# Kernel optimization log

Measured on AMD Instinct MI355X. Metric: run time of the kernel, lower is better.

Reference implementation:

```python
import jax, jax.numpy as jnp
import numpy as np

MODEL_DIM = 1024
HEADS = 16
HEAD_DIM = MODEL_DIM // HEADS
OUT_DIM = 1024
B, S = 2, 2048


def setup_inputs() -> dict:
    key = jax.random.key(0)
    ks = jax.random.split(key, 10)
    scale = 1.0 / np.sqrt(MODEL_DIM)
    return {
        "query": jax.random.normal(ks[0], (B, S, MODEL_DIM), dtype=jnp.float32),
        "bank": jax.random.normal(ks[1], (B, S, MODEL_DIM), dtype=jnp.float32),
        "Wq": jax.random.normal(ks[2], (MODEL_DIM, MODEL_DIM), dtype=jnp.float32) * scale,
        "bq": jnp.zeros((MODEL_DIM,), dtype=jnp.float32),
        "Wk": jax.random.normal(ks[3], (MODEL_DIM, MODEL_DIM), dtype=jnp.float32) * scale,
        "bk": jnp.zeros((MODEL_DIM,), dtype=jnp.float32),
        "Wv": jax.random.normal(ks[4], (MODEL_DIM, MODEL_DIM), dtype=jnp.float32) * scale,
        "bv": jnp.zeros((MODEL_DIM,), dtype=jnp.float32),
        "Wo": jax.random.normal(ks[5], (OUT_DIM, MODEL_DIM), dtype=jnp.float32) * scale,
        "bo": jnp.zeros((OUT_DIM,), dtype=jnp.float32),
    }


def _split_heads(x):
    # [B, S, D] -> [B, H, S, hd]
    b, s, _ = x.shape
    return x.reshape(b, s, HEADS, HEAD_DIM).transpose(0, 2, 1, 3)


def reference(query, bank, Wq, bq, Wk, bk, Wv, bv, Wo, bo):
    # Linear projections (torch Linear: x @ W.T + b)
    q = _split_heads(query @ Wq.T + bq)  # [B,H,Sq,hd]
    k = _split_heads(bank @ Wk.T + bk)   # [B,H,Sk,hd]
    v = _split_heads(bank @ Wv.T + bv)   # [B,H,Sk,hd]
    score_scale = jnp.sqrt(jnp.float32(HEAD_DIM))
    scores = jnp.einsum("bhqd,bhkd->bhqk", q / score_scale, k)  # [B,H,Sq,Sk]
    attn = jax.nn.softmax(scores, axis=-1)
    # dropout is identity in eval-mode reference
    ctx = jnp.einsum("bhqk,bhkd->bhqd", attn, v)  # [B,H,Sq,hd]
    b, h, sq, hd = ctx.shape
    ctx = ctx.transpose(0, 2, 1, 3).reshape(b, sq, MODEL_DIM)
    return ctx @ Wo.T + bo
```

## Files before the change

kernel.cpp:

```cpp
#include <hip/hip_runtime.h>


#define BDIM   2
#define SDIM   2048
#define DDIM   1024
#define HEADS  16
#define HD     64
#define MROWS  (BDIM * SDIM)

typedef float  f32x4  __attribute__((ext_vector_type(4)));
typedef __bf16 bf16x8 __attribute__((ext_vector_type(8)));
typedef __bf16 bf16x4 __attribute__((ext_vector_type(4)));
typedef unsigned u32x4 __attribute__((ext_vector_type(4)));

#define QSCALE 0.18033688011112042f

__device__ __forceinline__ void stage16(const void* g, void* l) {
    __builtin_amdgcn_global_load_lds((const __attribute__((address_space(1))) void*)g,
                                     (__attribute__((address_space(3))) void*)l,
                                     16, 0, 0);
}

__device__ __forceinline__ float vexp2(float x) {
    float r;
    asm("v_exp_f32 %0, %1" : "=v"(r) : "v"(x));
    return r;
}
__device__ __forceinline__ unsigned pk2(float lo, float hi) {
    unsigned r;
    asm("v_cvt_pk_bf16_f32 %0, %1, %2" : "=v"(r) : "v"(lo), "v"(hi));
    return r;
}

__global__ __launch_bounds__(256) void cvt_all(
    const float* __restrict__ q, const float* __restrict__ bank,
    const float* __restrict__ Wq, const float* __restrict__ Wk,
    const float* __restrict__ Wv, const float* __restrict__ Wo,
    __bf16* __restrict__ xq, __bf16* __restrict__ xkv,
    __bf16* __restrict__ wq, __bf16* __restrict__ wk,
    __bf16* __restrict__ wv, __bf16* __restrict__ wo) {
    const int i = blockIdx.x * 256 + threadIdx.x;
    const float* in;
    __bf16* out;
    int off;
    if (i < 524288)       { in = q;    out = xq;  off = i; }
    else if (i < 1048576) { in = bank; out = xkv; off = i - 524288; }
    else {
        const int j = i - 1048576;
        const int sel = j >> 17;
        off = j & 131071;
        in  = (sel == 0) ? Wq : (sel == 1) ? Wk : (sel == 2) ? Wv : Wo;
        out = (sel == 0) ? wq : (sel == 1) ? wk : (sel == 2) ? wv : wo;
    }
    const float4* p = (const float4*)in;
    float4 a = p[2 * off];
    float4 c = p[2 * off + 1];
    bf16x8 o;
    o[0] = (__bf16)a.x; o[1] = (__bf16)a.y; o[2] = (__bf16)a.z; o[3] = (__bf16)a.w;
    o[4] = (__bf16)c.x; o[5] = (__bf16)c.y; o[6] = (__bf16)c.z; o[7] = (__bf16)c.w;
    *(bf16x8*)(out + 8 * off) = o;
}

template <int MODE>
__global__ __launch_bounds__(256) void gemm_bt(
    const __bf16* __restrict__ Aq, const __bf16* __restrict__ Akv,
    const __bf16* __restrict__ W0, const __bf16* __restrict__ W1,
    const __bf16* __restrict__ W2,
    const float* __restrict__ b0, const float* __restrict__ b1,
    const float* __restrict__ b2,
    __bf16* __restrict__ Qo, __bf16* __restrict__ Ko, __bf16* __restrict__ Vo,
    float* __restrict__ Fo) {
    constexpr int NF = (MODE == 2) ? 2 : 4;
    constexpr int NCOL = NF * 32;
    __shared__ __align__(16) __bf16 ldsA[128 * 32];
    __shared__ __align__(16) __bf16 ldsB[(NCOL)*32];

    const int t = threadIdx.x;
    const int l = t & 63;
    const int w = t >> 6;
    const int z = (MODE == 0) ? (int)blockIdx.z : 0;

    const __bf16* A  = (MODE == 0 && z != 0) ? Akv : Aq;
    const __bf16* Wm = (z == 0) ? W0 : (z == 1 ? W1 : W2);
    const float*  bias = (z == 0) ? b0 : (z == 1 ? b1 : b2);

    const int row0 = blockIdx.x * 128;
    const int col0 = blockIdx.y * NCOL;

    const int sg = (t & 3) ^ ((t >> 3) & 3);
    const __bf16* ga = A  + (size_t)(row0 + (t >> 2)) * DDIM + sg * 8;
    const __bf16* gb = Wm + (size_t)(col0 + (t >> 2)) * DDIM + sg * 8;
    __bf16* la = ldsA + (t & ~63) * 8;
    __bf16* lb = ldsB + (t & ~63) * 8;

    const int wm = w >> 1, wn = w & 1;
    const int i15 = l & 15;
    const int q4 = l >> 4;
    const int gx = q4 ^ ((i15 >> 1) & 3);

    const int aoff = (wm * 64 + i15) * 32 + gx * 8;
    const int boff = (wn * (NF * 16) + i15) * 32 + gx * 8;

    f32x4 acc[4][NF] = {};

    for (int kb = 0; kb < DDIM; kb += 32) {
        __syncthreads();
        stage16(ga + kb,             la);
        stage16(ga + kb + 64 * DDIM, la + 2048);
        stage16(gb + kb,             lb);
        if constexpr (MODE == 0)
            stage16(gb + kb + 64 * DDIM, lb + 2048);
        __syncthreads();

        bf16x8 af[4], bf[NF];
#pragma unroll
        for (int m = 0; m < 4; ++m) af[m] = *(const bf16x8*)(ldsA + aoff + m * 16 * 32);
#pragma unroll
        for (int n = 0; n < NF; ++n) bf[n] = *(const bf16x8*)(ldsB + boff + n * 16 * 32);
#pragma unroll
        for (int m = 0; m < 4; ++m)
#pragma unroll
            for (int n = 0; n < NF; ++n)
                acc[m][n] = __builtin_amdgcn_mfma_f32_16x16x32_bf16(af[m], bf[n], acc[m][n], 0, 0, 0);
    }

#pragma unroll
    for (int m = 0; m < 4; ++m) {
        const int rbase = row0 + wm * 64 + m * 16 + (l >> 4) * 4;
#pragma unroll
        for (int n = 0; n < NF; ++n) {
            const int col = col0 + wn * (NF * 16) + n * 16 + (l & 15);
            const float bv = bias[col];
            if constexpr (MODE == 0) {
                const int hh = col >> 6, dd = col & 63;
#pragma unroll
                for (int j = 0; j < 4; ++j) {
                    const int r = rbase + j;
                    const int b = r >> 11, s = r & 2047;
                    const float v = acc[m][n][j] + bv;
                    if (z == 0) {
                        Qo[(((b * HEADS + hh) * SDIM + s) << 6) + dd] = (__bf16)(v * QSCALE);
                    } else if (z == 1) {
                        Ko[(((b * HEADS + hh) * SDIM + s) << 6) + dd] = (__bf16)v;
                    } else {
                        Vo[(((b * HEADS + hh) * HD + dd) << 11) + s] = (__bf16)v;
                    }
                }
            } else {
#pragma unroll
                for (int j = 0; j < 4; ++j) {
                    Fo[(size_t)(rbase + j) * DDIM + col] = acc[m][n][j] + bv;
                }
            }
        }
    }
}

__global__ __launch_bounds__(512) void attn_fwd(const __bf16* __restrict__ Qb,
                                                const __bf16* __restrict__ Kb,
                                                const __bf16* __restrict__ Vtb,
                                                __bf16* __restrict__ Cb) {
    __shared__ __align__(16) __bf16 ldsK[2][2][64 * 64];
    __shared__ __align__(16) __bf16 ldsV[2][2][64 * 64];

    const int t = threadIdx.x;
    const int l = t & 63;
    const int w = t >> 6;
    const int i15 = l & 15;
    const int q4 = l >> 4;

    const int bid  = blockIdx.x;
    const int xcd  = bid & 7;
    const int wloc = bid >> 3;
    const int bh   = xcd * 4 + (wloc >> 4);
    const int qb   = wloc & 15;
    const int b    = bh >> 4;
    const int h    = bh & 15;
    const size_t base = (size_t)bh * SDIM * HD;
    const int q0 = qb * 128;

    const __bf16* qp = Qb + base + (size_t)(q0 + w * 16 + i15) * HD + q4 * 8;
    const bf16x8 qf0 = *(const bf16x8*)(qp);
    const bf16x8 qf1 = *(const bf16x8*)(qp + 32);

    const int r0 = t >> 3;
    const int sl = (t & 7) ^ (r0 & 7);
    const int sig0 = ((r0 >> 5) << 5) | (((r0 >> 2) & 3) << 3)
                   | (((r0 >> 4) & 1) << 2) | (r0 & 3);
    const __bf16* gk = Kb  + base + (size_t)sig0 * HD + sl * 8;
    const __bf16* gv = Vtb + base + (size_t)r0 * SDIM + sl * 8;
    const int wb = (t & ~63) * 8;

    const int xr = i15 & 7;
    int off[4][2];
#pragma unroll
    for (int n = 0; n < 4; ++n)
#pragma unroll
        for (int hh = 0; hh < 2; ++hh)
            off[n][hh] = (n * 16 + i15) * 64 + (((hh * 4 + q4) ^ xr) << 3);

    bf16x8 ones;
#pragma unroll
    for (int j = 0; j < 8; ++j) ones[j] = (__bf16)1.0f;

    f32x4 c[4] = {};
    f32x4 lsum = {};

    stage16(gk,           &ldsK[0][0][wb]);
    stage16(gk + 64 * HD, &ldsK[0][1][wb]);
    stage16(gv,           &ldsV[0][0][wb]);
    stage16(gv + 64,      &ldsV[0][1][wb]);

#pragma unroll 2
    for (int r = 0; r < SDIM / 128; ++r) {
        const int bb = r & 1;
        __syncthreads();

        if (r + 1 < SDIM / 128) {
            const int s0 = (r + 1) * 128;
            stage16(gk + (size_t)s0 * HD,        &ldsK[bb ^ 1][0][wb]);
            stage16(gk + (size_t)(s0 + 64) * HD, &ldsK[bb ^ 1][1][wb]);
            stage16(gv + s0,                     &ldsV[bb ^ 1][0][wb]);
            stage16(gv + s0 + 64,                &ldsV[bb ^ 1][1][wb]);
        }

        const __bf16* lk0 = &ldsK[bb][0][0];
        const __bf16* lk1 = &ldsK[bb][1][0];
        const __bf16* lv0 = &ldsV[bb][0][0];
        const __bf16* lv1 = &ldsV[bb][1][0];

        f32x4 sA[4] = {}, sB[4] = {};
        __builtin_amdgcn_s_setprio(1);
#pragma unroll
        for (int n = 0; n < 4; ++n) {
            bf16x8 k0 = *(const bf16x8*)(lk0 + off[n][0]);
            bf16x8 k1 = *(const bf16x8*)(lk0 + off[n][1]);
            sA[n] = __builtin_amdgcn_mfma_f32_16x16x32_bf16(k0, qf0, sA[n], 0, 0, 0);
            sA[n] = __builtin_amdgcn_mfma_f32_16x16x32_bf16(k1, qf1, sA[n], 0, 0, 0);
        }
#pragma unroll
        for (int n = 0; n < 4; ++n) {
            bf16x8 k0 = *(const bf16x8*)(lk1 + off[n][0]);
            bf16x8 k1 = *(const bf16x8*)(lk1 + off[n][1]);
            sB[n] = __builtin_amdgcn_mfma_f32_16x16x32_bf16(k0, qf0, sB[n], 0, 0, 0);
            sB[n] = __builtin_amdgcn_mfma_f32_16x16x32_bf16(k1, qf1, sB[n], 0, 0, 0);
        }
        __builtin_amdgcn_s_setprio(0);

#pragma unroll
        for (int n = 0; n < 4; ++n)
#pragma unroll
            for (int j = 0; j < 4; ++j) {
                sA[n][j] = vexp2(sA[n][j]);
                sB[n][j] = vexp2(sB[n][j]);
            }

        u32x4 pw0, pw1, pw2, pw3;
        pw0[0] = pk2(sA[0][0], sA[0][1]); pw0[1] = pk2(sA[0][2], sA[0][3]);
        pw0[2] = pk2(sA[1][0], sA[1][1]); pw0[3] = pk2(sA[1][2], sA[1][3]);
        pw1[0] = pk2(sA[2][0], sA[2][1]); pw1[1] = pk2(sA[2][2], sA[2][3]);
        pw1[2] = pk2(sA[3][0], sA[3][1]); pw1[3] = pk2(sA[3][2], sA[3][3]);
        pw2[0] = pk2(sB[0][0], sB[0][1]); pw2[1] = pk2(sB[0][2], sB[0][3]);
        pw2[2] = pk2(sB[1][0], sB[1][1]); pw2[3] = pk2(sB[1][2], sB[1][3]);
        pw3[0] = pk2(sB[2][0], sB[2][1]); pw3[1] = pk2(sB[2][2], sB[2][3]);
        pw3[2] = pk2(sB[3][0], sB[3][1]); pw3[3] = pk2(sB[3][2], sB[3][3]);
        const bf16x8 paA0 = __builtin_bit_cast(bf16x8, pw0);
        const bf16x8 paB0 = __builtin_bit_cast(bf16x8, pw1);
        const bf16x8 paA1 = __builtin_bit_cast(bf16x8, pw2);
        const bf16x8 paB1 = __builtin_bit_cast(bf16x8, pw3);

        __builtin_amdgcn_s_setprio(1);
        lsum = __builtin_amdgcn_mfma_f32_16x16x32_bf16(ones, paA0, lsum, 0, 0, 0);
        lsum = __builtin_amdgcn_mfma_f32_16x16x32_bf16(ones, paB0, lsum, 0, 0, 0);
        lsum = __builtin_amdgcn_mfma_f32_16x16x32_bf16(ones, paA1, lsum, 0, 0, 0);
        lsum = __builtin_amdgcn_mfma_f32_16x16x32_bf16(ones, paB1, lsum, 0, 0, 0);
#pragma unroll
        for (int n2 = 0; n2 < 4; ++n2) {
            bf16x8 v0 = *(const bf16x8*)(lv0 + off[n2][0]);
            bf16x8 v1 = *(const bf16x8*)(lv0 + off[n2][1]);
            c[n2] = __builtin_amdgcn_mfma_f32_16x16x32_bf16(v0, paA0, c[n2], 0, 0, 0);
            c[n2] = __builtin_amdgcn_mfma_f32_16x16x32_bf16(v1, paB0, c[n2], 0, 0, 0);
            bf16x8 u0 = *(const bf16x8*)(lv1 + off[n2][0]);
            bf16x8 u1 = *(const bf16x8*)(lv1 + off[n2][1]);
            c[n2] = __builtin_amdgcn_mfma_f32_16x16x32_bf16(u0, paA1, c[n2], 0, 0, 0);
            c[n2] = __builtin_amdgcn_mfma_f32_16x16x32_bf16(u1, paB1, c[n2], 0, 0, 0);
        }
        __builtin_amdgcn_s_setprio(0);
    }

    const float inv = 1.0f / lsum[0];
    const int q = q0 + w * 16 + i15;
#pragma unroll
    for (int n2 = 0; n2 < 4; ++n2) {
        bf16x4 o;
#pragma unroll
        for (int j = 0; j < 4; ++j) o[j] = (__bf16)(c[n2][j] * inv);
        *(bf16x4*)(Cb + (size_t)(b * SDIM + q) * DDIM + h * HD + n2 * 16 + q4 * 4) = o;
    }
}

extern "C" void kernel_launch(void* const* d_in, const int* in_sizes, int n_in,
                              void* d_out, int out_size, void* d_ws, size_t ws_size,
                              hipStream_t stream) {
    const float* query = (const float*)d_in[0];
    const float* bank  = (const float*)d_in[1];
    const float* Wq = (const float*)d_in[2];
    const float* bq = (const float*)d_in[3];
    const float* Wk = (const float*)d_in[4];
    const float* bk = (const float*)d_in[5];
    const float* Wv = (const float*)d_in[6];
    const float* bv = (const float*)d_in[7];
    const float* Wo = (const float*)d_in[8];
    const float* bo = (const float*)d_in[9];
    float* out = (float*)d_out;

    char* ws = (char*)d_ws;
    __bf16* xq  = (__bf16*)(ws);
    __bf16* xkv = (__bf16*)(ws + (8u  << 20));
    __bf16* wq  = (__bf16*)(ws + (16u << 20));
    __bf16* wk  = (__bf16*)(ws + (18u << 20));
    __bf16* wv  = (__bf16*)(ws + (20u << 20));
    __bf16* wo  = (__bf16*)(ws + (22u << 20));
    __bf16* qbuf = (__bf16*)(ws + (24u << 20));
    __bf16* kbuf = (__bf16*)(ws + (32u << 20));
    __bf16* vtbuf = (__bf16*)(ws + (40u << 20));
    __bf16* ctx = xq;

    cvt_all<<<6144, 256, 0, stream>>>(query, bank, Wq, Wk, Wv, Wo,
                                      xq, xkv, wq, wk, wv, wo);

    gemm_bt<0><<<dim3(32, 8, 3), 256, 0, stream>>>(
        xq, xkv, wq, wk, wv, bq, bk, bv, qbuf, kbuf, vtbuf, nullptr);

    attn_fwd<<<512, 512, 0, stream>>>(qbuf, kbuf, vtbuf, ctx);

    gemm_bt<2><<<dim3(32, 16, 1), 256, 0, stream>>>(
        ctx, nullptr, wo, nullptr, nullptr, bo, nullptr, nullptr,
        nullptr, nullptr, nullptr, out);
}
```

Baseline: 112.4 us.

## Have each attention wave process two 16-row query tiles with half the threads

The attention kernel now launches 256 threads per block instead of 512. Each wave handles two 16-row query tiles (rows q and q+64), so every K and V fragment read from LDS feeds twice as many MFMAs. Staging is split into twice as many 16-byte loads per thread to fill the same 128-key tiles. This cuts LDS read traffic per unit of compute but doubles accumulator and score registers per wave and halves the waves per block, which may reduce latency hiding.

```diff
diff --git a/kernel.cpp b/kernel.cpp
--- a/kernel.cpp
+++ b/kernel.cpp
@@ -156,7 +156,7 @@
     }
 }
 
-__global__ __launch_bounds__(512) void attn_fwd(const __bf16* __restrict__ Qb,
+__global__ __launch_bounds__(256) void attn_fwd(const __bf16* __restrict__ Qb,
                                                 const __bf16* __restrict__ Kb,
                                                 const __bf16* __restrict__ Vtb,
                                                 __bf16* __restrict__ Cb) {
@@ -180,13 +180,14 @@
     const int q0 = qb * 128;
 
     const __bf16* qp = Qb + base + (size_t)(q0 + w * 16 + i15) * HD + q4 * 8;
-    const bf16x8 qf0 = *(const bf16x8*)(qp);
-    const bf16x8 qf1 = *(const bf16x8*)(qp + 32);
+    const bf16x8 qf00 = *(const bf16x8*)(qp);
+    const bf16x8 qf01 = *(const bf16x8*)(qp + 32);
+    const bf16x8 qf10 = *(const bf16x8*)(qp + 64 * HD);
+    const bf16x8 qf11 = *(const bf16x8*)(qp + 64 * HD + 32);
 
     const int r0 = t >> 3;
     const int sl = (t & 7) ^ (r0 & 7);
-    const int sig0 = ((r0 >> 5) << 5) | (((r0 >> 2) & 3) << 3)
-                   | (((r0 >> 4) & 1) << 2) | (r0 & 3);
+    const int sig0 = (((r0 >> 2) & 3) << 3) | (((r0 >> 4) & 1) << 2) | (r0 & 3);
     const __bf16* gk = Kb  + base + (size_t)sig0 * HD + sl * 8;
     const __bf16* gv = Vtb + base + (size_t)r0 * SDIM + sl * 8;
     const int wb = (t & ~63) * 8;
@@ -203,13 +204,17 @@
 #pragma unroll
     for (int j = 0; j < 8; ++j) ones[j] = (__bf16)1.0f;
 
-    f32x4 c[4] = {};
-    f32x4 lsum = {};
-
-    stage16(gk,           &ldsK[0][0][wb]);
-    stage16(gk + 64 * HD, &ldsK[0][1][wb]);
-    stage16(gv,           &ldsV[0][0][wb]);
-    stage16(gv + 64,      &ldsV[0][1][wb]);
+    f32x4 c0[4] = {}, c1[4] = {};
+    f32x4 ls0 = {}, ls1 = {};
+
+    stage16(gk,                       &ldsK[0][0][wb]);
+    stage16(gk + 32 * HD,             &ldsK[0][0][wb + 2048]);
+    stage16(gk + 64 * HD,             &ldsK[0][1][wb]);
+    stage16(gk + 96 * HD,             &ldsK[0][1][wb + 2048]);
+    stage16(gv,                       &ldsV[0][0][wb]);
+    stage16(gv + (size_t)32 * SDIM,   &ldsV[0][0][wb + 2048]);
+    stage16(gv + 64,                  &ldsV[0][1][wb]);
+    stage16(gv + 64 + (size_t)32 * SDIM, &ldsV[0][1][wb + 2048]);
 
 #pragma unroll 2
     for (int r = 0; r < SDIM / 128; ++r) {
@@ -218,10 +223,14 @@
 
         if (r + 1 < SDIM / 128) {
             const int s0 = (r + 1) * 128;
-            stage16(gk + (size_t)s0 * HD,        &ldsK[bb ^ 1][0][wb]);
-            stage16(gk + (size_t)(s0 + 64) * HD, &ldsK[bb ^ 1][1][wb]);
-            stage16(gv + s0,                     &ldsV[bb ^ 1][0][wb]);
-            stage16(gv + s0 + 64,                &ldsV[bb ^ 1][1][wb]);
+            stage16(gk + (size_t)(s0)*HD,          &ldsK[bb ^ 1][0][wb]);
+            stage16(gk + (size_t)(s0 + 32) * HD,   &ldsK[bb ^ 1][0][wb + 2048]);
+            stage16(gk + (size_t)(s0 + 64) * HD,   &ldsK[bb ^ 1][1][wb]);
+            stage16(gk + (size_t)(s0 + 96) * HD,   &ldsK[bb ^ 1][1][wb + 2048]);
+            stage16(gv + s0,                       &ldsV[bb ^ 1][0][wb]);
+            stage16(gv + s0 + (size_t)32 * SDIM,   &ldsV[bb ^ 1][0][wb + 2048]);
+            stage16(gv + s0 + 64,                  &ldsV[bb ^ 1][1][wb]);
+            stage16(gv + s0 + 64 + (size_t)32 * SDIM, &ldsV[bb ^ 1][1][wb + 2048]);
         }
 
         const __bf16* lk0 = &ldsK[bb][0][0];
@@ -229,21 +238,25 @@
         const __bf16* lv0 = &ldsV[bb][0][0];
         const __bf16* lv1 = &ldsV[bb][1][0];
 
-        f32x4 sA[4] = {}, sB[4] = {};
+        f32x4 sA[4] = {}, sB[4] = {}, sC[4] = {}, sD[4] = {};
         __builtin_amdgcn_s_setprio(1);
 #pragma unroll
         for (int n = 0; n < 4; ++n) {
             bf16x8 k0 = *(const bf16x8*)(lk0 + off[n][0]);
             bf16x8 k1 = *(const bf16x8*)(lk0 + off[n][1]);
-            sA[n] = __builtin_amdgcn_mfma_f32_16x16x32_bf16(k0, qf0, sA[n], 0, 0, 0);
-            sA[n] = __builtin_amdgcn_mfma_f32_16x16x32_bf16(k1, qf1, sA[n], 0, 0, 0);
+            sA[n] = __builtin_amdgcn_mfma_f32_16x16x32_bf16(k0, qf00, sA[n], 0, 0, 0);
+            sC[n] = __builtin_amdgcn_mfma_f32_16x16x32_bf16(k0, qf10, sC[n], 0, 0, 0);
+            sA[n] = __builtin_amdgcn_mfma_f32_16x16x32_bf16(k1, qf01, sA[n], 0, 0, 0);
+            sC[n] = __builtin_amdgcn_mfma_f32_16x16x32_bf16(k1, qf11, sC[n], 0, 0, 0);
         }
 #pragma unroll
         for (int n = 0; n < 4; ++n) {
             bf16x8 k0 = *(const bf16x8*)(lk1 + off[n][0]);
             bf16x8 k1 = *(const bf16x8*)(lk1 + off[n][1]);
-            sB[n] = __builtin_amdgcn_mfma_f32_16x16x32_bf16(k0, qf0, sB[n], 0, 0, 0);
-            sB[n] = __builtin_amdgcn_mfma_f32_16x16x32_bf16(k1, qf1, sB[n], 0, 0, 0);
+            sB[n] = __builtin_amdgcn_mfma_f32_16x16x32_bf16(k0, qf00, sB[n], 0, 0, 0);
+            sD[n] = __builtin_amdgcn_mfma_f32_16x16x32_bf16(k0, qf10, sD[n], 0, 0, 0);
+            sB[n] = __builtin_amdgcn_mfma_f32_16x16x32_bf16(k1, qf01, sB[n], 0, 0, 0);
+            sD[n] = __builtin_amdgcn_mfma_f32_16x16x32_bf16(k1, qf11, sD[n], 0, 0, 0);
         }
         __builtin_amdgcn_s_setprio(0);
 
@@ -253,49 +266,76 @@
             for (int j = 0; j < 4; ++j) {
                 sA[n][j] = vexp2(sA[n][j]);
                 sB[n][j] = vexp2(sB[n][j]);
+                sC[n][j] = vexp2(sC[n][j]);
+                sD[n][j] = vexp2(sD[n][j]);
             }
 
-        u32x4 pw0, pw1, pw2, pw3;
-        pw0[0] = pk2(sA[0][0], sA[0][1]); pw0[1] = pk2(sA[0][2], sA[0][3]);
-        pw0[2] = pk2(sA[1][0], sA[1][1]); pw0[3] = pk2(sA[1][2], sA[1][3]);
-        pw1[0] = pk2(sA[2][0], sA[2][1]); pw1[1] = pk2(sA[2][2], sA[2][3]);
-        pw1[2] = pk2(sA[3][0], sA[3][1]); pw1[3] = pk2(sA[3][2], sA[3][3]);
-        pw2[0] = pk2(sB[0][0], sB[0][1]); pw2[1] = pk2(sB[0][2], sB[0][3]);
-        pw2[2] = pk2(sB[1][0], sB[1][1]); pw2[3] = pk2(sB[1][2], sB[1][3]);
-        pw3[0] = pk2(sB[2][0], sB[2][1]); pw3[1] = pk2(sB[2][2], sB[2][3]);
-        pw3[2] = pk2(sB[3][0], sB[3][1]); pw3[3] = pk2(sB[3][2], sB[3][3]);
-        const bf16x8 paA0 = __builtin_bit_cast(bf16x8, pw0);
-        const bf16x8 paB0 = __builtin_bit_cast(bf16x8, pw1);
-        const bf16x8 paA1 = __builtin_bit_cast(bf16x8, pw2);
-        const bf16x8 paB1 = __builtin_bit_cast(bf16x8, pw3);
+        u32x4 w0, w1, w2, w3, w4, w5, w6, w7;
+        w0[0] = pk2(sA[0][0], sA[0][1]); w0[1] = pk2(sA[0][2], sA[0][3]);
+        w0[2] = pk2(sA[1][0], sA[1][1]); w0[3] = pk2(sA[1][2], sA[1][3]);
+        w1[0] = pk2(sA[2][0], sA[2][1]); w1[1] = pk2(sA[2][2], sA[2][3]);
+        w1[2] = pk2(sA[3][0], sA[3][1]); w1[3] = pk2(sA[3][2], sA[3][3]);
+        w2[0] = pk2(sB[0][0], sB[0][1]); w2[1] = pk2(sB[0][2], sB[0][3]);
+        w2[2] = pk2(sB[1][0], sB[1][1]); w2[3] = pk2(sB[1][2], sB[1][3]);
+        w3[0] = pk2(sB[2][0], sB[2][1]); w3[1] = pk2(sB[2][2], sB[2][3]);
+        w3[2] = pk2(sB[3][0], sB[3][1]); w3[3] = pk2(sB[3][2], sB[3][3]);
+        w4[0] = pk2(sC[0][0], sC[0][1]); w4[1] = pk2(sC[0][2], sC[0][3]);
+        w4[2] = pk2(sC[1][0], sC[1][1]); w4[3] = pk2(sC[1][2], sC[1][3]);
+        w5[0] = pk2(sC[2][0], sC[2][1]); w5[1] = pk2(sC[2][2], sC[2][3]);
+        w5[2] = pk2(sC[3][0], sC[3][1]); w5[3] = pk2(sC[3][2], sC[3][3]);
+        w6[0] = pk2(sD[0][0], sD[0][1]); w6[1] = pk2(sD[0][2], sD[0][3]);
+        w6[2] = pk2(sD[1][0], sD[1][1]); w6[3] = pk2(sD[1][2], sD[1][3]);
+        w7[0] = pk2(sD[2][0], sD[2][1]); w7[1] = pk2(sD[2][2], sD[2][3]);
+        w7[2] = pk2(sD[3][0], sD[3][1]); w7[3] = pk2(sD[3][2], sD[3][3]);
+        const bf16x8 pA = __builtin_bit_cast(bf16x8, w0);
+        const bf16x8 pB = __builtin_bit_cast(bf16x8, w1);
+        const bf16x8 pC = __builtin_bit_cast(bf16x8, w2);
+        const bf16x8 pD = __builtin_bit_cast(bf16x8, w3);
+        const bf16x8 rA = __builtin_bit_cast(bf16x8, w4);
+        const bf16x8 rB = __builtin_bit_cast(bf16x8, w5);
+        const bf16x8 rC = __builtin_bit_cast(bf16x8, w6);
+        const bf16x8 rD = __builtin_bit_cast(bf16x8, w7);
 
         __builtin_amdgcn_s_setprio(1);
-        lsum = __builtin_amdgcn_mfma_f32_16x16x32_bf16(ones, paA0, lsum, 0, 0, 0);
-        lsum = __builtin_amdgcn_mfma_f32_16x16x32_bf16(ones, paB0, lsum, 0, 0, 0);
-        lsum = __builtin_amdgcn_mfma_f32_16x16x32_bf16(ones, paA1, lsum, 0, 0, 0);
-        lsum = __builtin_amdgcn_mfma_f32_16x16x32_bf16(ones, paB1, lsum, 0, 0, 0);
+        ls0 = __builtin_amdgcn_mfma_f32_16x16x32_bf16(ones, pA, ls0, 0, 0, 0);
+        ls0 = __builtin_amdgcn_mfma_f32_16x16x32_bf16(ones, pB, ls0, 0, 0, 0);
+        ls0 = __builtin_amdgcn_mfma_f32_16x16x32_bf16(ones, pC, ls0, 0, 0, 0);
+        ls0 = __builtin_amdgcn_mfma_f32_16x16x32_bf16(ones, pD, ls0, 0, 0, 0);
+        ls1 = __builtin_amdgcn_mfma_f32_16x16x32_bf16(ones, rA, ls1, 0, 0, 0);
+        ls1 = __builtin_amdgcn_mfma_f32_16x16x32_bf16(ones, rB, ls1, 0, 0, 0);
+        ls1 = __builtin_amdgcn_mfma_f32_16x16x32_bf16(ones, rC, ls1, 0, 0, 0);
+        ls1 = __builtin_amdgcn_mfma_f32_16x16x32_bf16(ones, rD, ls1, 0, 0, 0);
 #pragma unroll
         for (int n2 = 0; n2 < 4; ++n2) {
             bf16x8 v0 = *(const bf16x8*)(lv0 + off[n2][0]);
             bf16x8 v1 = *(const bf16x8*)(lv0 + off[n2][1]);
-            c[n2] = __builtin_amdgcn_mfma_f32_16x16x32_bf16(v0, paA0, c[n2], 0, 0, 0);
-            c[n2] = __builtin_amdgcn_mfma_f32_16x16x32_bf16(v1, paB0, c[n2], 0, 0, 0);
+            c0[n2] = __builtin_amdgcn_mfma_f32_16x16x32_bf16(v0, pA, c0[n2], 0, 0, 0);
+            c1[n2] = __builtin_amdgcn_mfma_f32_16x16x32_bf16(v0, rA, c1[n2], 0, 0, 0);
+            c0[n2] = __builtin_amdgcn_mfma_f32_16x16x32_bf16(v1, pB, c0[n2], 0, 0, 0);
+            c1[n2] = __builtin_amdgcn_mfma_f32_16x16x32_bf16(v1, rB, c1[n2], 0, 0, 0);
             bf16x8 u0 = *(const bf16x8*)(lv1 + off[n2][0]);
             bf16x8 u1 = *(const bf16x8*)(lv1 + off[n2][1]);
-            c[n2] = __builtin_amdgcn_mfma_f32_16x16x32_bf16(u0, paA1, c[n2], 0, 0, 0);
-            c[n2] = __builtin_amdgcn_mfma_f32_16x16x32_bf16(u1, paB1, c[n2], 0, 0, 0);
+            c0[n2] = __builtin_amdgcn_mfma_f32_16x16x32_bf16(u0, pC, c0[n2], 0, 0, 0);
+            c1[n2] = __builtin_amdgcn_mfma_f32_16x16x32_bf16(u0, rC, c1[n2], 0, 0, 0);
+            c0[n2] = __builtin_amdgcn_mfma_f32_16x16x32_bf16(u1, pD, c0[n2], 0, 0, 0);
+            c1[n2] = __builtin_amdgcn_mfma_f32_16x16x32_bf16(u1, rD, c1[n2], 0, 0, 0);
         }
         __builtin_amdgcn_s_setprio(0);
     }
 
-    const float inv = 1.0f / lsum[0];
+    const float inv0 = 1.0f / ls0[0];
+    const float inv1 = 1.0f / ls1[0];
     const int q = q0 + w * 16 + i15;
 #pragma unroll
     for (int n2 = 0; n2 < 4; ++n2) {
-        bf16x4 o;
-#pragma unroll
-        for (int j = 0; j < 4; ++j) o[j] = (__bf16)(c[n2][j] * inv);
-        *(bf16x4*)(Cb + (size_t)(b * SDIM + q) * DDIM + h * HD + n2 * 16 + q4 * 4) = o;
+        bf16x4 oA, oB;
+#pragma unroll
+        for (int j = 0; j < 4; ++j) {
+            oA[j] = (__bf16)(c0[n2][j] * inv0);
+            oB[j] = (__bf16)(c1[n2][j] * inv1);
+        }
+        *(bf16x4*)(Cb + (size_t)(b * SDIM + q) * DDIM + h * HD + n2 * 16 + q4 * 4) = oA;
+        *(bf16x4*)(Cb + (size_t)(b * SDIM + q + 64) * DDIM + h * HD + n2 * 16 + q4 * 4) = oB;
     }
 }
 
@@ -332,7 +372,7 @@
     gemm_bt<0><<<dim3(32, 8, 3), 256, 0, stream>>>(
         xq, xkv, wq, wk, wv, bq, bk, bv, qbuf, kbuf, vtbuf, nullptr);
 
-    attn_fwd<<<512, 512, 0, stream>>>(qbuf, kbuf, vtbuf, ctx);
+    attn_fwd<<<512, 256, 0, stream>>>(qbuf, kbuf, vtbuf, ctx);
 
     gemm_bt<2><<<dim3(32, 16, 1), 256, 0, stream>>>(
         ctx, nullptr, wo, nullptr, nullptr, bo, nullptr, nullptr,
```

Measured after the change: 112.2 us. No clear change (-0.1%).

## Fuse fp32-to-bf16 activation conversion into QKV projection GEMM

Applied to the files above, without the earlier changes.

The standalone pass that converted query and bank activations to bf16 is removed. The QKV GEMM now stages fp32 activation tiles straight into LDS with a new swizzle and packs them to bf16 in registers before the MFMA. Only the weights are still pre-converted. This avoids a full read and write of both activation tensors, at the cost of twice the LDS footprint and staging traffic for the A operand plus extra pack instructions, and the z=1 and z=2 blocks each re-read the fp32 bank.

```diff
diff --git a/kernel.cpp b/kernel.cpp
--- a/kernel.cpp
+++ b/kernel.cpp
@@ -32,38 +32,31 @@
     return r;
 }
 
-__global__ __launch_bounds__(256) void cvt_all(
-    const float* __restrict__ q, const float* __restrict__ bank,
-    const float* __restrict__ Wq, const float* __restrict__ Wk,
-    const float* __restrict__ Wv, const float* __restrict__ Wo,
-    __bf16* __restrict__ xq, __bf16* __restrict__ xkv,
-    __bf16* __restrict__ wq, __bf16* __restrict__ wk,
-    __bf16* __restrict__ wv, __bf16* __restrict__ wo) {
-    const int i = blockIdx.x * 256 + threadIdx.x;
-    const float* in;
-    __bf16* out;
-    int off;
-    if (i < 524288)       { in = q;    out = xq;  off = i; }
-    else if (i < 1048576) { in = bank; out = xkv; off = i - 524288; }
-    else {
-        const int j = i - 1048576;
-        const int sel = j >> 17;
-        off = j & 131071;
-        in  = (sel == 0) ? Wq : (sel == 1) ? Wk : (sel == 2) ? Wv : Wo;
-        out = (sel == 0) ? wq : (sel == 1) ? wk : (sel == 2) ? wv : wo;
-    }
+__global__ __launch_bounds__(256) void cvt8w(const float* __restrict__ w0,
+                                             const float* __restrict__ w1,
+                                             const float* __restrict__ w2,
+                                             const float* __restrict__ w3,
+                                             __bf16* __restrict__ o0,
+                                             __bf16* __restrict__ o1,
+                                             __bf16* __restrict__ o2,
+                                             __bf16* __restrict__ o3) {
+    const int sel = blockIdx.x >> 9;
+    const float* in  = (sel == 0) ? w0 : (sel == 1) ? w1 : (sel == 2) ? w2 : w3;
+    __bf16*      out = (sel == 0) ? o0 : (sel == 1) ? o1 : (sel == 2) ? o2 : o3;
+    int i = (blockIdx.x & 511) * 256 + threadIdx.x;
     const float4* p = (const float4*)in;
-    float4 a = p[2 * off];
-    float4 c = p[2 * off + 1];
+    float4 a = p[2 * i];
+    float4 c = p[2 * i + 1];
     bf16x8 o;
     o[0] = (__bf16)a.x; o[1] = (__bf16)a.y; o[2] = (__bf16)a.z; o[3] = (__bf16)a.w;
     o[4] = (__bf16)c.x; o[5] = (__bf16)c.y; o[6] = (__bf16)c.z; o[7] = (__bf16)c.w;
-    *(bf16x8*)(out + 8 * off) = o;
+    *(bf16x8*)(out + 8 * i) = o;
 }
 
 template <int MODE>
 __global__ __launch_bounds__(256) void gemm_bt(
-    const __bf16* __restrict__ Aq, const __bf16* __restrict__ Akv,
+    const float* __restrict__ Fq, const float* __restrict__ Fkv,
+    const __bf16* __restrict__ Ab,
     const __bf16* __restrict__ W0, const __bf16* __restrict__ W1,
     const __bf16* __restrict__ W2,
     const float* __restrict__ b0, const float* __restrict__ b1,
@@ -72,51 +65,91 @@
     float* __restrict__ Fo) {
     constexpr int NF = (MODE == 2) ? 2 : 4;
     constexpr int NCOL = NF * 32;
-    __shared__ __align__(16) __bf16 ldsA[128 * 32];
-    __shared__ __align__(16) __bf16 ldsB[(NCOL)*32];
+    constexpr int ABYTES = (MODE == 0) ? (128 * 32 * 4) : (128 * 32 * 2);
+    __shared__ __align__(16) char ldsAraw[ABYTES];
+    __shared__ __align__(16) __bf16 ldsB[NCOL * 32];
 
     const int t = threadIdx.x;
     const int l = t & 63;
     const int w = t >> 6;
     const int z = (MODE == 0) ? (int)blockIdx.z : 0;
 
-    const __bf16* A  = (MODE == 0 && z != 0) ? Akv : Aq;
     const __bf16* Wm = (z == 0) ? W0 : (z == 1 ? W1 : W2);
     const float*  bias = (z == 0) ? b0 : (z == 1 ? b1 : b2);
 
     const int row0 = blockIdx.x * 128;
     const int col0 = blockIdx.y * NCOL;
 
-    const int sg = (t & 3) ^ ((t >> 3) & 3);
-    const __bf16* ga = A  + (size_t)(row0 + (t >> 2)) * DDIM + sg * 8;
-    const __bf16* gb = Wm + (size_t)(col0 + (t >> 2)) * DDIM + sg * 8;
-    __bf16* la = ldsA + (t & ~63) * 8;
+    const int sgB = (t & 3) ^ ((t >> 3) & 3);
+    const __bf16* gb = Wm + (size_t)(col0 + (t >> 2)) * DDIM + sgB * 8;
     __bf16* lb = ldsB + (t & ~63) * 8;
 
     const int wm = w >> 1, wn = w & 1;
     const int i15 = l & 15;
     const int q4 = l >> 4;
-    const int gx = q4 ^ ((i15 >> 1) & 3);
-
-    const int aoff = (wm * 64 + i15) * 32 + gx * 8;
-    const int boff = (wn * (NF * 16) + i15) * 32 + gx * 8;
+    const int gxB = q4 ^ ((i15 >> 1) & 3);
+
+    int boff[NF];
+#pragma unroll
+    for (int n = 0; n < NF; ++n)
+        boff[n] = (wn * (NF * 16) + n * 16 + i15) * 32 + gxB * 8;
+
+    float*  ldsAf = (float*)ldsAraw;
+    __bf16* ldsAb = (__bf16*)ldsAraw;
+
+    const float* Af = (z == 0) ? Fq : Fkv;
+    const int sgAf = (t & 7) ^ ((t >> 3) & 7);
+    const float* gaf = (MODE == 0) ? (Af + (size_t)(row0 + (t >> 3)) * DDIM + sgAf * 4) : nullptr;
+    float* laf = ldsAf + (t & ~63) * 4;
+
+    const __bf16* gab = (MODE == 2) ? (Ab + (size_t)(row0 + (t >> 2)) * DDIM + sgB * 8) : nullptr;
+    __bf16* lab = ldsAb + (t & ~63) * 8;
+
+    const int xrA = i15 & 7;
+    int ao0[4], ao1[4], aob[4];
+#pragma unroll
+    for (int m = 0; m < 4; ++m) {
+        const int row = wm * 64 + m * 16 + i15;
+        ao0[m] = row * 32 + (((2 * q4) ^ xrA) << 2);
+        ao1[m] = row * 32 + (((2 * q4 + 1) ^ xrA) << 2);
+        aob[m] = row * 32 + gxB * 8;
+    }
 
     f32x4 acc[4][NF] = {};
 
     for (int kb = 0; kb < DDIM; kb += 32) {
         __syncthreads();
-        stage16(ga + kb,             la);
-        stage16(ga + kb + 64 * DDIM, la + 2048);
-        stage16(gb + kb,             lb);
+        if constexpr (MODE == 0) {
+            stage16(gaf + kb,             laf);
+            stage16(gaf + kb + 32 * DDIM, laf + 1024);
+            stage16(gaf + kb + 64 * DDIM, laf + 2048);
+            stage16(gaf + kb + 96 * DDIM, laf + 3072);
+        } else {
+            stage16(gab + kb,             lab);
+            stage16(gab + kb + 64 * DDIM, lab + 2048);
+        }
+        stage16(gb + kb, lb);
         if constexpr (MODE == 0)
             stage16(gb + kb + 64 * DDIM, lb + 2048);
         __syncthreads();
 
         bf16x8 af[4], bf[NF];
-#pragma unroll
-        for (int m = 0; m < 4; ++m) af[m] = *(const bf16x8*)(ldsA + aoff + m * 16 * 32);
-#pragma unroll
-        for (int n = 0; n < NF; ++n) bf[n] = *(const bf16x8*)(ldsB + boff + n * 16 * 32);
+        if constexpr (MODE == 0) {
+#pragma unroll
+            for (int m = 0; m < 4; ++m) {
+                f32x4 a0 = *(const f32x4*)(ldsAf + ao0[m]);
+                f32x4 a1 = *(const f32x4*)(ldsAf + ao1[m]);
+                u32x4 wa;
+                wa[0] = pk2(a0[0], a0[1]); wa[1] = pk2(a0[2], a0[3]);
+                wa[2] = pk2(a1[0], a1[1]); wa[3] = pk2(a1[2], a1[3]);
+                af[m] = __builtin_bit_cast(bf16x8, wa);
+            }
+        } else {
+#pragma unroll
+            for (int m = 0; m < 4; ++m) af[m] = *(const bf16x8*)(ldsAb + aob[m]);
+        }
+#pragma unroll
+        for (int n = 0; n < NF; ++n) bf[n] = *(const bf16x8*)(ldsB + boff[n]);
 #pragma unroll
         for (int m = 0; m < 4; ++m)
 #pragma unroll
@@ -315,8 +348,7 @@
     float* out = (float*)d_out;
 
     char* ws = (char*)d_ws;
-    __bf16* xq  = (__bf16*)(ws);
-    __bf16* xkv = (__bf16*)(ws + (8u  << 20));
+    __bf16* ctx = (__bf16*)(ws);
     __bf16* wq  = (__bf16*)(ws + (16u << 20));
     __bf16* wk  = (__bf16*)(ws + (18u << 20));
     __bf16* wv  = (__bf16*)(ws + (20u << 20));
@@ -324,17 +356,15 @@
     __bf16* qbuf = (__bf16*)(ws + (24u << 20));
     __bf16* kbuf = (__bf16*)(ws + (32u << 20));
     __bf16* vtbuf = (__bf16*)(ws + (40u << 20));
-    __bf16* ctx = xq;
-
-    cvt_all<<<6144, 256, 0, stream>>>(query, bank, Wq, Wk, Wv, Wo,
-                                      xq, xkv, wq, wk, wv, wo);
+
+    cvt8w<<<2048, 256, 0, stream>>>(Wq, Wk, Wv, Wo, wq, wk, wv, wo);
 
     gemm_bt<0><<<dim3(32, 8, 3), 256, 0, stream>>>(
-        xq, xkv, wq, wk, wv, bq, bk, bv, qbuf, kbuf, vtbuf, nullptr);
+        query, bank, nullptr, wq, wk, wv, bq, bk, bv, qbuf, kbuf, vtbuf, nullptr);
 
     attn_fwd<<<512, 512, 0, stream>>>(qbuf, kbuf, vtbuf, ctx);
 
     gemm_bt<2><<<dim3(32, 16, 1), 256, 0, stream>>>(
-        ctx, nullptr, wo, nullptr, nullptr, bo, nullptr, nullptr,
+        nullptr, nullptr, ctx, wo, nullptr, nullptr, bo, nullptr, nullptr,
         nullptr, nullptr, nullptr, out);
 }
```

New measurement: 113.0 us. About the same (+0.6%).
